# Performance work log

Hardware: AMD Instinct MI355X
Metric: run time of the kernel (lower is better)

Reference implementation:

```python
import math
import jax, jax.numpy as jnp
import numpy as np

N_NODES = 50000
N_EDGES = 400000
DIM = 64
HEADS = 4
GAMMA = 1.0
SIC_STRENGTH = 0.5


def _n2n(x):
    return jnp.nan_to_num(x, nan=0.0, posinf=0.0, neginf=0.0)


def _n2n_c(z):
    return jax.lax.complex(_n2n(z.real), _n2n(z.imag))


def setup_inputs() -> dict:
    key = jax.random.key(0)
    ks = jax.random.split(key, 8)
    scale = 1.0 / math.sqrt(DIM)  # ComplexLinear uniform(-1/sqrt(fan_in), 1/sqrt(fan_in))
    h_real = jax.random.normal(ks[0], (N_NODES, DIM), dtype=jnp.float32)
    h_imag = jax.random.normal(ks[1], (N_NODES, DIM), dtype=jnp.float32)
    W_real = jax.random.uniform(ks[2], (HEADS, DIM, DIM), minval=-scale, maxval=scale, dtype=jnp.float32)
    W_imag = jax.random.uniform(ks[3], (HEADS, DIM, DIM), minval=-scale, maxval=scale, dtype=jnp.float32)
    Q_real = jax.random.uniform(ks[4], (HEADS, DIM, DIM), minval=-scale, maxval=scale, dtype=jnp.float32)
    Q_imag = jax.random.uniform(ks[5], (HEADS, DIM, DIM), minval=-scale, maxval=scale, dtype=jnp.float32)
    msg_gate_raw = jnp.full((1,), 0.5, dtype=jnp.float32)  # _msg_gate init
    modrelu_b = jnp.zeros((DIM,), dtype=jnp.float32)
    src = jax.random.randint(ks[6], (N_EDGES,), 0, N_NODES, dtype=jnp.int32)
    dst = jax.random.randint(ks[7], (N_EDGES,), 0, N_NODES, dtype=jnp.int32)
    return {"h_real": h_real, "h_imag": h_imag, "W_real": W_real, "W_imag": W_imag,
            "Q_real": Q_real, "Q_imag": Q_imag, "msg_gate_raw": msg_gate_raw,
            "modrelu_b": modrelu_b, "src": src, "dst": dst}


def _segment_softmax(logits, seg, num_segments):
    # torch_geometric softmax: exp(x - max_seg) / (sum_seg + 1e-16)
    seg_max = jax.ops.segment_max(logits, seg, num_segments=num_segments)
    ex = jnp.exp(logits - seg_max[seg])
    denom = jax.ops.segment_sum(ex, seg, num_segments=num_segments)[seg] + 1e-16
    return ex / denom


def _forward(h_real, h_imag, W_real, W_imag, Q_real, Q_imag, msg_gate_raw, modrelu_b, src, dst):
    h = jax.lax.complex(h_real, h_imag)              # [N, D] complex64
    N, D = h.shape
    hs = h[src]                                      # [E, D] gather src
    hd = h[dst]                                      # [E, D] gather dst
    norm2 = jnp.clip(jnp.sum(hd.real ** 2 + hd.imag ** 2, axis=1, keepdims=True), 1e-6, None)
    gate = jax.nn.sigmoid(msg_gate_raw[0])

    # cosine similarity of real parts (detached), torch eps = 1e-8
    eps = 1e-8
    na = jnp.maximum(jnp.linalg.norm(hs.real, axis=-1), eps)
    nb = jnp.maximum(jnp.linalg.norm(hd.real, axis=-1), eps)
    sim = jnp.clip(jnp.sum(hs.real * hd.real, axis=-1) / (na * nb), -1.0, 1.0)
    sign = jax.lax.stop_gradient(jnp.sign(sim))      # [E]
    sign_gate = (0.5 + 0.5 * sign)[:, None]          # real factor applied to complex base

    updates = jnp.zeros((N, D), dtype=h.dtype)
    inv_sqrt_d = 1.0 / math.sqrt(D)
    for m in range(W_real.shape[0]):
        Wm = jax.lax.complex(W_real[m], W_imag[m])   # [D_out, D_in]
        Qm = jax.lax.complex(Q_real[m], Q_imag[m])
        Wh = _n2n_c(hs @ Wm.T)                       # transported, [E, D]
        dot = _n2n_c(jnp.sum(jnp.conj(hd) * Wh, axis=1, keepdims=True))
        proj = _n2n_c(hd * (dot / norm2))
        r = _n2n_c(Wh - SIC_STRENGTH * proj)
        Qh = _n2n_c(hd @ Qm.T)
        s = _n2n_c(jnp.sum(jnp.conj(Qh) * r, axis=1))
        logits = _n2n(GAMMA * jnp.abs(s) * inv_sqrt_d)
        alpha = _n2n(_segment_softmax(logits, dst, N))  # dropout is identity in eval
        base = _n2n_c((gate * r + (1.0 - gate) * Wh) * sign_gate)
        msg = _n2n_c(alpha[:, None] * base)
        updates = updates.at[dst].add(msg)

    h_new = _n2n_c(h + updates)
    # NodeNorm on view_as_real: mean/std over feature axis (dim=-2 of [N, D, 2]), ddof=1
    xr = jnp.stack([h_new.real, h_new.imag], axis=-1)          # [N, D, 2]
    mean = jnp.mean(xr, axis=-2, keepdims=True)
    std = jnp.clip(jnp.std(xr, axis=-2, ddof=1, keepdims=True), 1e-5, None)
    xn = _n2n((xr - mean) / std)
    h_new = jax.lax.complex(xn[..., 0], xn[..., 1])
    # ModReLU
    mag = jnp.clip(jnp.abs(h_new), 1e-6, None)
    gated = jax.nn.relu(mag + modrelu_b)
    out = _n2n_c(gated * (h_new / mag))
    return jnp.stack([out.real, out.imag], axis=-1)            # [N, D, 2] real view


def reference(h_real, h_imag, W_real, W_imag, Q_real, Q_imag, msg_gate_raw, modrelu_b, src, dst):
    return _forward(h_real, h_imag, W_real, W_imag, Q_real, Q_imag, msg_gate_raw, modrelu_b, src, dst)
```

## Files before the change

### kernel.cpp

```cpp
#include <hip/hip_runtime.h>
#include <hip/hip_bf16.h>
#include <math.h>

#define NN 50000
#define NE 400000
#define DIM 64
#define HEADS 4
#define SIC 0.5f
#define NBLK ((NN + 255) / 256)

typedef _Float16 f16x8 __attribute__((ext_vector_type(8)));
typedef _Float16 f16x2 __attribute__((ext_vector_type(2)));
typedef float f32x4 __attribute__((ext_vector_type(4)));

__device__ __forceinline__ unsigned pack_f16c(float re, float im) {
    f16x2 p; p[0] = (_Float16)re; p[1] = (_Float16)im;
    return __builtin_bit_cast(unsigned, p);
}

__device__ __forceinline__ f16x2 swapneg(f16x2 v) {
    unsigned u = __builtin_bit_cast(unsigned, v);
    u = ((u >> 16) | (u << 16)) ^ 0x8000u;
    return __builtin_bit_cast(f16x2, u);
}

__device__ __forceinline__ float dpp_red8(float x) {
    int xi = __builtin_bit_cast(int, x);
    x += __builtin_bit_cast(float, __builtin_amdgcn_update_dpp(0, xi, 0xB1, 0xF, 0xF, true));
    xi = __builtin_bit_cast(int, x);
    x += __builtin_bit_cast(float, __builtin_amdgcn_update_dpp(0, xi, 0x4E, 0xF, 0xF, true));
    xi = __builtin_bit_cast(int, x);
    x += __builtin_bit_cast(float, __builtin_amdgcn_update_dpp(0, xi, 0x141, 0xF, 0xF, true));
    return x;
}
__device__ __forceinline__ float dpp_red16(float x) {
    x = dpp_red8(x);
    int xi = __builtin_bit_cast(int, x);
    x += __builtin_bit_cast(float, __builtin_amdgcn_update_dpp(0, xi, 0x140, 0xF, 0xF, true));
    return x;
}

#define SA (512 * 128)
#define SB (SA + 512 * 128)
#define SC (SB + 128 * 512)
#define SD (SC + NN * 64)
#define SE (SD + NE)
__global__ void k_pre(const float* __restrict__ h_re, const float* __restrict__ h_im,
                      const float* __restrict__ Wre, const float* __restrict__ Wim,
                      const float* __restrict__ Qre, const float* __restrict__ Qim,
                      const int* __restrict__ dst,
                      _Float16* __restrict__ BtQ, _Float16* __restrict__ BtWH,
                      _Float16* __restrict__ B2f, unsigned* __restrict__ P16,
                      int* __restrict__ counts) {
    int tid = blockIdx.x * blockDim.x + threadIdx.x;
    if (tid < SA) {
        int c = tid >> 7, k = tid & 127;
        int mh = c >> 7, cm = c & 127;
        int comp = cm >> 6, o = cm & 63;
        int i = k >> 1, cin = k & 1;
        int widx = (mh * DIM + o) * DIM + i;
        float v;
        if (cin == 0) v = comp ? Qim[widx] : Qre[widx];
        else          v = comp ? Qre[widx] : -Qim[widx];
        BtQ[tid] = (_Float16)v;
    } else if (tid < SB) {
        int t2 = tid - SA;
        int c = t2 >> 7, k = t2 & 127;
        int mh = c >> 7, cm = c & 127;
        int comp = cm >> 6, o = cm & 63;
        int i = k >> 1, cin = k & 1;
        int widx = (mh * DIM + i) * DIM + o;
        float v;
        if (cin == 0) v = comp ? -Wim[widx] : Wre[widx];
        else          v = comp ?  Wre[widx] : Wim[widx];
        BtWH[t2] = (_Float16)v;
    } else if (tid < SC) {
        int t2 = tid - SB;
        int c_out = t2 >> 9, k = t2 & 511;
        int comp_out = c_out >> 6, o = c_out & 63;
        int m = k >> 7, cin = k & 1, i = (k >> 1) & 63;
        int widx = (m * DIM + o) * DIM + i;
        float v;
        if (cin == 0) v = comp_out ? Wim[widx] : Wre[widx];
        else          v = comp_out ? Wre[widx] : -Wim[widx];
        B2f[t2] = (_Float16)v;
    } else if (tid < SD) {
        int t2 = tid - SC;
        int n = t2 >> 6, d = t2 & 63;
        P16[t2] = pack_f16c(h_re[n * 64 + d], h_im[n * 64 + d]);
    } else if (tid < SE) {
        int e = tid - SD;
        atomicAdd(&counts[dst[e]], 1);
    }
}

__global__ __launch_bounds__(256) void k1f(
    const unsigned* __restrict__ P16, const _Float16* __restrict__ BtQ,
    const _Float16* __restrict__ BtWH, unsigned* __restrict__ W16) {
    __shared__ unsigned Qy[256 * 68];
    int b = blockIdx.x;
    int mh = b & 3, chunk = b >> 2;
    int w = threadIdx.x >> 6, l = threadIdx.x & 63;
    int r = l & 15, g = l >> 4;
    int nbase = chunk * 256;
    const _Float16* A = (const _Float16*)P16;

    {
        f16x8 Wf[2][4];
#pragma unroll
        for (int t = 0; t < 2; ++t)
#pragma unroll
            for (int ch = 0; ch < 4; ++ch)
                Wf[t][ch] = *(const f16x8*)(BtQ + (mh * 128 + t * 64 + w * 16 + r) * 128 + ch * 32 + g * 8);

        f16x8 N[3][4];
#pragma unroll
        for (int p = 0; p < 2; ++p) {
            int nc = min(nbase + p * 16 + r, NN - 1);
#pragma unroll
            for (int ch = 0; ch < 4; ++ch)
                N[p][ch] = *(const f16x8*)(A + (size_t)nc * 128 + ch * 32 + g * 8);
        }

#pragma unroll
        for (int nt = 0; nt < 16; ++nt) {
            const int cur = nt % 3;
            if (nt + 2 < 16) {
                const int nxt = (nt + 2) % 3;
                int nc = min(nbase + (nt + 2) * 16 + r, NN - 1);
#pragma unroll
                for (int ch = 0; ch < 4; ++ch)
                    N[nxt][ch] = *(const f16x8*)(A + (size_t)nc * 128 + ch * 32 + g * 8);
            }
            f32x4 a0 = {0.f, 0.f, 0.f, 0.f}, a1 = {0.f, 0.f, 0.f, 0.f};
#pragma unroll
            for (int ch = 0; ch < 4; ++ch) {
                a0 = __builtin_amdgcn_mfma_f32_16x16x32_f16(Wf[0][ch], N[cur][ch], a0, 0, 0, 0);
                a1 = __builtin_amdgcn_mfma_f32_16x16x32_f16(Wf[1][ch], N[cur][ch], a1, 0, 0, 0);
            }
            uint4 u;
            u.x = pack_f16c(a0[0], a1[0]);
            u.y = pack_f16c(a0[1], a1[1]);
            u.z = pack_f16c(a0[2], a1[2]);
            u.w = pack_f16c(a0[3], a1[3]);
            int node = nt * 16 + r;
            *(uint4*)&Qy[node * 68 + w * 16 + g * 4] = u;
        }
    }
    __syncthreads();

#pragma unroll 4
    for (int it = 0; it < 16; ++it) {
        int node = it * 16 + w * 4 + (l >> 4);
        int ll = l & 15, d0 = ll * 4;
        int n_glob = nbase + node;
        uint4 q = *(const uint4*)&Qy[node * 68 + d0];
        uint4 hp = make_uint4(0, 0, 0, 0);
        if (n_glob < NN) hp = *(const uint4*)&P16[(size_t)n_glob * 64 + d0];
        unsigned qw[4] = {q.x, q.y, q.z, q.w};
        unsigned hw[4] = {hp.x, hp.y, hp.z, hp.w};
        float qre[4], qim[4], hre[4], him[4];
        float tr = 0.f, ti = 0.f, n2 = 0.f;
#pragma unroll
        for (int j = 0; j < 4; ++j) {
            f16x2 pq = __builtin_bit_cast(f16x2, qw[j]);
            f16x2 ph = __builtin_bit_cast(f16x2, hw[j]);
            qre[j] = (float)pq[0]; qim[j] = (float)pq[1];
            hre[j] = (float)ph[0]; him[j] = (float)ph[1];
            tr += qre[j] * hre[j] + qim[j] * him[j];
            ti += qre[j] * him[j] - qim[j] * hre[j];
            n2 += hre[j] * hre[j] + him[j] * him[j];
        }
        tr = dpp_red16(tr); ti = dpp_red16(ti); n2 = dpp_red16(n2);
        float cfac = SIC / fmaxf(n2, 1e-6f);
        float kre = cfac * tr, kim = cfac * ti;
        uint4 y;
        unsigned* yp = &y.x;
#pragma unroll
        for (int j = 0; j < 4; ++j) {
            float yre = qre[j] - (kre * hre[j] + kim * him[j]);
            float yim = qim[j] - (kre * him[j] - kim * hre[j]);
            yp[j] = pack_f16c(yre, yim);
        }
        *(uint4*)&Qy[node * 68 + d0] = y;
    }
    __syncthreads();

    {
        f16x8 Wf[2][4];
#pragma unroll
        for (int t = 0; t < 2; ++t)
#pragma unroll
            for (int ch = 0; ch < 4; ++ch)
                Wf[t][ch] = *(const f16x8*)(BtWH + (mh * 128 + t * 64 + w * 16 + r) * 128 + ch * 32 + g * 8);

#pragma unroll
        for (int nt = 0; nt < 16; ++nt) {
            f32x4 a0 = {0.f, 0.f, 0.f, 0.f}, a1 = {0.f, 0.f, 0.f, 0.f};
#pragma unroll
            for (int ch = 0; ch < 4; ++ch) {
                f16x8 nf = *(const f16x8*)&Qy[(nt * 16 + r) * 68 + ch * 16 + g * 4];
                a0 = __builtin_amdgcn_mfma_f32_16x16x32_f16(Wf[0][ch], nf, a0, 0, 0, 0);
                a1 = __builtin_amdgcn_mfma_f32_16x16x32_f16(Wf[1][ch], nf, a1, 0, 0, 0);
            }
            int n = nbase + nt * 16 + r;
            if (n < NN) {
                uint4 u;
                u.x = pack_f16c(a0[0], a1[0]);
                u.y = pack_f16c(a0[1], a1[1]);
                u.z = pack_f16c(a0[2], a1[2]);
                u.w = pack_f16c(a0[3], a1[3]);
                *(uint4*)&W16[((size_t)n * 4 + mh) * 64 + w * 16 + g * 4] = u;
            }
        }
    }
}

__global__ __launch_bounds__(256) void k2b1(const int* __restrict__ counts,
                                            int* __restrict__ bsum) {
    __shared__ int red[256];
    int t = threadIdx.x;
    int i = blockIdx.x * 256 + t;
    red[t] = (i < NN) ? counts[i] : 0;
    __syncthreads();
    for (int off = 128; off; off >>= 1) {
        if (t < off) red[t] += red[t + off];
        __syncthreads();
    }
    if (t == 0) bsum[blockIdx.x] = red[0];
}

__global__ __launch_bounds__(256) void k2b2(const int* __restrict__ bsum,
                                            int* __restrict__ bpre) {
    __shared__ int buf[256];
    int t = threadIdx.x;
    int v = (t < NBLK) ? bsum[t] : 0;
    buf[t] = v;
    __syncthreads();
    for (int off = 1; off < 256; off <<= 1) {
        int x = 0;
        if (t >= off) x = buf[t - off];
        __syncthreads();
        buf[t] += x;
        __syncthreads();
    }
    if (t < NBLK) bpre[t] = buf[t] - v;
}

__global__ __launch_bounds__(256) void k2b3(const int* __restrict__ counts,
                                            const int* __restrict__ bpre,
                                            int* __restrict__ row_ptr, int* __restrict__ cursor) {
    __shared__ int buf[256];
    int t = threadIdx.x;
    int i = blockIdx.x * 256 + t;
    int v = (i < NN) ? counts[i] : 0;
    buf[t] = v;
    __syncthreads();
    for (int off = 1; off < 256; off <<= 1) {
        int x = 0;
        if (t >= off) x = buf[t - off];
        __syncthreads();
        buf[t] += x;
        __syncthreads();
    }
    int excl = buf[t] - v + bpre[blockIdx.x];
    if (i < NN) { row_ptr[i] = excl; cursor[i] = excl; }
    if (i == NN - 1) row_ptr[NN] = excl + v;
}

__global__ void k2c_fill(const int* __restrict__ src, const int* __restrict__ dst,
                         int* __restrict__ cursor, int* __restrict__ sorted_src) {
    int e = blockIdx.x * blockDim.x + threadIdx.x;
    if (e < NE) {
        int pos = atomicAdd(&cursor[dst[e]], 1);
        sorted_src[pos] = src[e] << 8;
    }
}

__global__ __launch_bounds__(128) void k_main(
    const float* __restrict__ h_re,
    const unsigned* __restrict__ P16,
    const unsigned* __restrict__ W16,
    const int* __restrict__ row_ptr, const int* __restrict__ sorted_src,
    _Float16* __restrict__ Sb) {
    int wave = threadIdx.x >> 6;
    int lane = threadIdx.x & 63;
    int n = blockIdx.x * 2 + wave;
    int e = lane >> 5;
    int g = (lane >> 3) & 3;
    int l = lane & 7;
    int d0 = l * 8;

    const char* hb = (const char*)h_re + d0 * 4;
    const char* pb = (const char*)P16 + d0 * 4;

    float hre[8];
    f16x2 w2[8], wn2[8];
    {
        float4 a0 = *(const float4*)(h_re + n * DIM + d0);
        float4 a1 = *(const float4*)(h_re + n * DIM + d0 + 4);
        hre[0] = a0.x; hre[1] = a0.y; hre[2] = a0.z; hre[3] = a0.w;
        hre[4] = a1.x; hre[5] = a1.y; hre[6] = a1.z; hre[7] = a1.w;
        const unsigned* wp = W16 + ((size_t)n * 4 + g) * 64 + d0;
        uint4 wa = *(const uint4*)wp, wb = *(const uint4*)(wp + 4);
        unsigned ww[8] = {wa.x, wa.y, wa.z, wa.w, wb.x, wb.y, wb.z, wb.w};
#pragma unroll
        for (int j = 0; j < 8; ++j) {
            w2[j] = __builtin_bit_cast(f16x2, ww[j]);
            wn2[j] = swapneg(w2[j]);
        }
    }

    int beg = row_ptr[n], end = row_ptr[n + 1];
    float l_run = 0.f;
    f16x2 ps[8];
#pragma unroll
    for (int j = 0; j < 8; ++j) ps[j] = f16x2{(_Float16)0.f, (_Float16)0.f};

    float4 aR0 = make_float4(0, 0, 0, 0), aR1 = aR0, bR0 = aR0, bR1 = aR0;
    uint4 aP0 = make_uint4(0, 0, 0, 0), aP1 = aP0, bP0 = aP0, bP1 = aP0;
    auto ldE = [&](int idx, float4& r0_, float4& r1_, uint4& p0_, uint4& p1_) {
        int soff = sorted_src[idx];
        r0_ = *(const float4*)(hb + soff);
        r1_ = *(const float4*)(hb + soff + 16);
        p0_ = *(const uint4*)(pb + soff);
        p1_ = *(const uint4*)(pb + soff + 16);
    };
    auto process = [&](const float4& R0, const float4& R1, const uint4& P0, const uint4& P1,
                       bool valid) {
        float csr[8] = {R0.x, R0.y, R0.z, R0.w, R1.x, R1.y, R1.z, R1.w};
        unsigned pw[8] = {P0.x, P0.y, P0.z, P0.w, P1.x, P1.y, P1.z, P1.w};
        float r2 = 0, r3 = 0, r4 = 0;
#pragma unroll
        for (int j = 0; j < 8; ++j) {
            f16x2 hs2 = __builtin_bit_cast(f16x2, pw[j]);
            r2 = __builtin_amdgcn_fdot2(w2[j], hs2, r2, false);
            r3 = __builtin_amdgcn_fdot2(wn2[j], hs2, r3, false);
            r4 = fmaf(hre[j], csr[j], r4);
        }
        r2 = dpp_red8(r2); r3 = dpp_red8(r3); r4 = dpp_red8(r4);

        float sg = (r4 > 0.f) ? 1.f : ((r4 < 0.f) ? 0.f : 0.5f);
        float mag2 = sqrtf(r2 * r2 + r3 * r3) * 0.180336880f;
        float ex = valid ? __builtin_exp2f(mag2) : 0.f;
        float wgt = fminf(ex * sg, 30000.f);
        l_run += ex;
        _Float16 wh = (_Float16)wgt;
        f16x2 wv = {wh, wh};
#pragma unroll
        for (int j = 0; j < 8; ++j) {
            f16x2 hs2 = __builtin_bit_cast(f16x2, pw[j]);
            ps[j] = ps[j] + wv * hs2;
        }
    };

    if (beg + e < end) ldE(beg + e, aR0, aR1, aP0, aP1);
    if (beg + 2 + e < end) ldE(beg + 2 + e, bR0, bR1, bP0, bP1);

    for (int pos = beg; pos < end; pos += 4) {
        process(aR0, aR1, aP0, aP1, (pos + e) < end);
        if (pos + 4 + e < end) ldE(pos + 4 + e, aR0, aR1, aP0, aP1);
        else { aR0 = make_float4(0, 0, 0, 0); aR1 = aR0; aP0 = make_uint4(0, 0, 0, 0); aP1 = aP0; }
        if (pos + 2 >= end) break;
        process(bR0, bR1, bP0, bP1, (pos + 2 + e) < end);
        if (pos + 6 + e < end) ldE(pos + 6 + e, bR0, bR1, bP0, bP1);
        else { bR0 = make_float4(0, 0, 0, 0); bR1 = bR0; bP0 = make_uint4(0, 0, 0, 0); bP1 = bP0; }
    }

#pragma unroll
    for (int j = 0; j < 8; ++j) {
        unsigned o = __shfl_xor(__builtin_bit_cast(unsigned, ps[j]), 32, 64);
        ps[j] = ps[j] + __builtin_bit_cast(f16x2, o);
    }
    l_run += __shfl_xor(l_run, 32, 64);

    float inv = (l_run > 0.f) ? (1.0f / l_run) : 0.f;
    if (e == 0) {
        _Float16 ih = (_Float16)inv;
        f16x2 iv = {ih, ih};
        uint4 o0, o1;
        unsigned* op0 = &o0.x;
        unsigned* op1 = &o1.x;
#pragma unroll
        for (int j = 0; j < 4; ++j) {
            op0[j] = __builtin_bit_cast(unsigned, (f16x2)(ps[j] * iv));
            op1[j] = __builtin_bit_cast(unsigned, (f16x2)(ps[j + 4] * iv));
        }
        _Float16* sp = Sb + (size_t)n * 512 + g * 128 + d0 * 2;
        *(uint4*)sp = o0;
        *(uint4*)(sp + 8) = o1;
    }
}

__global__ __launch_bounds__(256) void k5_ws(
    const float* __restrict__ h_re, const float* __restrict__ h_im,
    const _Float16* __restrict__ Sb,
    const _Float16* __restrict__ B2f,
    const float* __restrict__ gate_raw, const float* __restrict__ modrelu_b,
    float2* __restrict__ out) {
    int w = threadIdx.x >> 6, l = threadIdx.x & 63;
    int n0 = blockIdx.x * 64 + w * 16;
    if (n0 >= NN) return;
    int r = l & 15, g = l >> 4;
    int nodeA = min(n0 + r, NN - 1);

    f16x8 A_[16];
#pragma unroll
    for (int ch = 0; ch < 16; ++ch)
        A_[ch] = *(const f16x8*)(Sb + (size_t)nodeA * 512 + ch * 32 + g * 8);

    f16x8 Bf[8];
#pragma unroll
    for (int nt = 0; nt < 8; ++nt)
        Bf[nt] = *(const f16x8*)(B2f + (nt * 16 + r) * 512 + g * 8);

    f32x4 acc[8];
#pragma unroll
    for (int t = 0; t < 8; ++t) acc[t] = {0.f, 0.f, 0.f, 0.f};

#pragma unroll
    for (int ch = 0; ch < 16; ++ch) {
#pragma unroll
        for (int nt = 0; nt < 8; ++nt) {
            f16x8 b = Bf[nt];
            if (ch + 1 < 16)
                Bf[nt] = *(const f16x8*)(B2f + (nt * 16 + r) * 512 + (ch + 1) * 32 + g * 8);
            acc[nt] = __builtin_amdgcn_mfma_f32_16x16x32_f16(A_[ch], b, acc[nt], 0, 0, 0);
        }
    }

    float gate = 1.0f / (1.0f + expf(-gate_raw[0]));
    float bo[4];
#pragma unroll
    for (int q = 0; q < 4; ++q) bo[q] = modrelu_b[q * 16 + r];

#pragma unroll
    for (int j = 0; j < 4; ++j) {
        int n = n0 + g * 4 + j;
        int nc = min(n, NN - 1);
        float hrv[4], hiv[4];
        float tsr = 0.f, tsi = 0.f, hn2 = 0.f;
#pragma unroll
        for (int q = 0; q < 4; ++q) {
            int o = q * 16 + r;
            hrv[q] = h_re[nc * DIM + o];
            hiv[q] = h_im[nc * DIM + o];
            tsr += hrv[q] * acc[q][j] + hiv[q] * acc[q + 4][j];
            tsi += hrv[q] * acc[q + 4][j] - hiv[q] * acc[q][j];
            hn2 += hrv[q] * hrv[q] + hiv[q] * hiv[q];
        }
#pragma unroll
        for (int off = 1; off < 16; off <<= 1) {
            tsr += __shfl_xor(tsr, off, 64);
            tsi += __shfl_xor(tsi, off, 64);
            hn2 += __shfl_xor(hn2, off, 64);
        }
        float cfac = gate * SIC / fmaxf(hn2, 1e-6f);
        float Tsr = cfac * tsr, Tsi = cfac * tsi;

        float xr_[4], xi_[4];
        float sr = 0.f, si = 0.f, qr = 0.f, qi = 0.f;
#pragma unroll
        for (int q = 0; q < 4; ++q) {
            float hr = hrv[q], hi = hiv[q];
            float nre = hr + acc[q][j]     - (Tsr * hr - Tsi * hi);
            float nim = hi + acc[q + 4][j] - (Tsr * hi + Tsi * hr);
            xr_[q] = nre; xi_[q] = nim;
            sr += nre; si += nim; qr += nre * nre; qi += nim * nim;
        }
#pragma unroll
        for (int off = 1; off < 16; off <<= 1) {
            sr += __shfl_xor(sr, off, 64);
            si += __shfl_xor(si, off, 64);
            qr += __shfl_xor(qr, off, 64);
            qi += __shfl_xor(qi, off, 64);
        }
        float mean_r = sr * (1.f / DIM), mean_i = si * (1.f / DIM);
        float var_r = (qr - DIM * mean_r * mean_r) * (1.f / (DIM - 1));
        float var_i = (qi - DIM * mean_i * mean_i) * (1.f / (DIM - 1));
        float std_r = fmaxf(sqrtf(fmaxf(var_r, 0.f)), 1e-5f);
        float std_i = fmaxf(sqrtf(fmaxf(var_i, 0.f)), 1e-5f);
        if (n < NN) {
#pragma unroll
            for (int q = 0; q < 4; ++q) {
                float xr = (xr_[q] - mean_r) / std_r;
                float xi = (xi_[q] - mean_i) / std_i;
                float mag = fmaxf(sqrtf(xr * xr + xi * xi), 1e-6f);
                float gg = fmaxf(mag + bo[q], 0.f);
                float sc = gg / mag;
                out[n * DIM + q * 16 + r] = make_float2(xr * sc, xi * sc);
            }
        }
    }
}

extern "C" void kernel_launch(void* const* d_in, const int* in_sizes, int n_in,
                              void* d_out, int out_size, void* d_ws, size_t ws_size,
                              hipStream_t stream) {
    const float* h_re = (const float*)d_in[0];
    const float* h_im = (const float*)d_in[1];
    const float* W_re = (const float*)d_in[2];
    const float* W_im = (const float*)d_in[3];
    const float* Q_re = (const float*)d_in[4];
    const float* Q_im = (const float*)d_in[5];
    const float* gate_raw = (const float*)d_in[6];
    const float* b = (const float*)d_in[7];
    const int* src = (const int*)d_in[8];
    const int* dst = (const int*)d_in[9];

    char* ws = (char*)d_ws;
    size_t off = 0;
    auto alloc = [&](size_t bytes) {
        void* p = ws + off;
        off = (off + bytes + 255) & ~(size_t)255;
        return p;
    };
    _Float16* Sb = (_Float16*)alloc((size_t)NN * 512 * sizeof(_Float16));
    _Float16* BtQ = (_Float16*)alloc((size_t)512 * 128 * sizeof(_Float16));
    _Float16* BtWH = (_Float16*)alloc((size_t)512 * 128 * sizeof(_Float16));
    _Float16* B2f = (_Float16*)alloc((size_t)128 * 512 * sizeof(_Float16));
    unsigned* P16 = (unsigned*)alloc((size_t)NN * 64 * sizeof(unsigned));
    unsigned* W16 = (unsigned*)alloc((size_t)NN * 256 * sizeof(unsigned));
    int* counts = (int*)alloc((size_t)NN * sizeof(int));
    int* row_ptr = (int*)alloc((size_t)(NN + 1) * sizeof(int));
    int* cursor = (int*)alloc((size_t)NN * sizeof(int));
    int* sorted_src = (int*)alloc((size_t)NE * sizeof(int));
    int* bsum = (int*)alloc((size_t)NBLK * sizeof(int));
    int* bpre = (int*)alloc((size_t)(NBLK + 1) * sizeof(int));

    hipMemsetAsync(counts, 0, (size_t)NN * sizeof(int), stream);
    k_pre<<<(SE + 255) / 256, 256, 0, stream>>>(h_re, h_im, W_re, W_im, Q_re, Q_im, dst,
                                                BtQ, BtWH, B2f, P16, counts);
    k1f<<<4 * NBLK, 256, 0, stream>>>(P16, BtQ, BtWH, W16);
    k2b1<<<NBLK, 256, 0, stream>>>(counts, bsum);
    k2b2<<<1, 256, 0, stream>>>(bsum, bpre);
    k2b3<<<NBLK, 256, 0, stream>>>(counts, bpre, row_ptr, cursor);
    k2c_fill<<<(NE + 255) / 256, 256, 0, stream>>>(src, dst, cursor, sorted_src);
    k_main<<<NN / 2, 128, 0, stream>>>(h_re, P16, W16, row_ptr, sorted_src, Sb);
    k5_ws<<<(NN + 63) / 64, 256, 0, stream>>>(h_re, h_im, Sb, B2f, gate_raw, b, (float2*)d_out);
}
```

Measured before the change: 262.0 us.

## Split k5 output columns across wave pairs and pre-swizzle B2 for coalesced loads

```diff
diff --git a/kernel.cpp b/kernel.cpp
--- a/kernel.cpp
+++ b/kernel.cpp
@@ -50,7 +50,7 @@
                       const float* __restrict__ Qre, const float* __restrict__ Qim,
                       const int* __restrict__ dst,
                       _Float16* __restrict__ BtQ, _Float16* __restrict__ BtWH,
-                      _Float16* __restrict__ B2f, unsigned* __restrict__ P16,
+                      _Float16* __restrict__ B2c, unsigned* __restrict__ P16,
                       int* __restrict__ counts) {
     int tid = blockIdx.x * blockDim.x + threadIdx.x;
     if (tid < SA) {
@@ -76,14 +76,20 @@
         BtWH[t2] = (_Float16)v;
     } else if (tid < SC) {
         int t2 = tid - SB;
-        int c_out = t2 >> 9, k = t2 & 511;
+        int ch = t2 >> 12;
+        int rem = t2 & 4095;
+        int nt = rem >> 9;
+        int rem2 = rem & 511;
+        int slot = rem2 >> 3, j = rem2 & 7;
+        int c_out = nt * 16 + (slot >> 2);
+        int k = ch * 32 + (slot & 3) * 8 + j;
         int comp_out = c_out >> 6, o = c_out & 63;
         int m = k >> 7, cin = k & 1, i = (k >> 1) & 63;
         int widx = (m * DIM + o) * DIM + i;
         float v;
         if (cin == 0) v = comp_out ? Wim[widx] : Wre[widx];
         else          v = comp_out ? Wre[widx] : -Wim[widx];
-        B2f[t2] = (_Float16)v;
+        B2c[t2] = (_Float16)v;
     } else if (tid < SD) {
         int t2 = tid - SC;
         int n = t2 >> 6, d = t2 & 63;
@@ -395,59 +401,77 @@
 __global__ __launch_bounds__(256) void k5_ws(
     const float* __restrict__ h_re, const float* __restrict__ h_im,
     const _Float16* __restrict__ Sb,
-    const _Float16* __restrict__ B2f,
+    const _Float16* __restrict__ B2c,
     const float* __restrict__ gate_raw, const float* __restrict__ modrelu_b,
     float2* __restrict__ out) {
+    __shared__ float xch[2][32][8];
     int w = threadIdx.x >> 6, l = threadIdx.x & 63;
-    int n0 = blockIdx.x * 64 + w * 16;
-    if (n0 >= NN) return;
     int r = l & 15, g = l >> 4;
+    int nh = w >> 1, ct = w & 1;
+    int nbase = blockIdx.x * 32;
+    int n0 = nbase + nh * 16;
     int nodeA = min(n0 + r, NN - 1);
-
-    f16x8 A_[16];
-#pragma unroll
-    for (int ch = 0; ch < 16; ++ch)
-        A_[ch] = *(const f16x8*)(Sb + (size_t)nodeA * 512 + ch * 32 + g * 8);
-
-    f16x8 Bf[8];
-#pragma unroll
-    for (int nt = 0; nt < 8; ++nt)
-        Bf[nt] = *(const f16x8*)(B2f + (nt * 16 + r) * 512 + g * 8);
-
-    f32x4 acc[8];
-#pragma unroll
-    for (int t = 0; t < 8; ++t) acc[t] = {0.f, 0.f, 0.f, 0.f};
-
+    int q0 = 2 * ct;
+    const int nt_[4] = {q0, q0 + 1, 4 + q0, 5 + q0};
+    int slot8 = ((r << 2) + g) << 3;
+
+    const _Float16* abase = Sb + (size_t)nodeA * 512 + g * 8;
+    const _Float16* bbase = B2c + slot8;
+
+    f32x4 acc[4];
+#pragma unroll
+    for (int t = 0; t < 4; ++t) acc[t] = {0.f, 0.f, 0.f, 0.f};
+
+    f16x8 Ac = *(const f16x8*)(abase);
+    f16x8 Bc0 = *(const f16x8*)(bbase + nt_[0] * 512);
+    f16x8 Bc1 = *(const f16x8*)(bbase + nt_[1] * 512);
+    f16x8 Bc2 = *(const f16x8*)(bbase + nt_[2] * 512);
+    f16x8 Bc3 = *(const f16x8*)(bbase + nt_[3] * 512);
 #pragma unroll
     for (int ch = 0; ch < 16; ++ch) {
-#pragma unroll
-        for (int nt = 0; nt < 8; ++nt) {
-            f16x8 b = Bf[nt];
-            if (ch + 1 < 16)
-                Bf[nt] = *(const f16x8*)(B2f + (nt * 16 + r) * 512 + (ch + 1) * 32 + g * 8);
-            acc[nt] = __builtin_amdgcn_mfma_f32_16x16x32_f16(A_[ch], b, acc[nt], 0, 0, 0);
-        }
+        f16x8 An = Ac, Bn0 = Bc0, Bn1 = Bc1, Bn2 = Bc2, Bn3 = Bc3;
+        if (ch + 1 < 16) {
+            An = *(const f16x8*)(abase + (ch + 1) * 32);
+            const _Float16* bn = bbase + (ch + 1) * 4096;
+            Bn0 = *(const f16x8*)(bn + nt_[0] * 512);
+            Bn1 = *(const f16x8*)(bn + nt_[1] * 512);
+            Bn2 = *(const f16x8*)(bn + nt_[2] * 512);
+            Bn3 = *(const f16x8*)(bn + nt_[3] * 512);
+        }
+        acc[0] = __builtin_amdgcn_mfma_f32_16x16x32_f16(Ac, Bc0, acc[0], 0, 0, 0);
+        acc[1] = __builtin_amdgcn_mfma_f32_16x16x32_f16(Ac, Bc1, acc[1], 0, 0, 0);
+        acc[2] = __builtin_amdgcn_mfma_f32_16x16x32_f16(Ac, Bc2, acc[2], 0, 0, 0);
+        acc[3] = __builtin_amdgcn_mfma_f32_16x16x32_f16(Ac, Bc3, acc[3], 0, 0, 0);
+        Ac = An; Bc0 = Bn0; Bc1 = Bn1; Bc2 = Bn2; Bc3 = Bn3;
     }
 
     float gate = 1.0f / (1.0f + expf(-gate_raw[0]));
-    float bo[4];
-#pragma unroll
-    for (int q = 0; q < 4; ++q) bo[q] = modrelu_b[q * 16 + r];
-
+    float bo[2];
+#pragma unroll
+    for (int qq = 0; qq < 2; ++qq) bo[qq] = modrelu_b[(q0 + qq) * 16 + r];
+
+    float hr[4][2], hi[4][2];
 #pragma unroll
     for (int j = 0; j < 4; ++j) {
-        int n = n0 + g * 4 + j;
-        int nc = min(n, NN - 1);
-        float hrv[4], hiv[4];
+        int nc = min(n0 + g * 4 + j, NN - 1);
+#pragma unroll
+        for (int qq = 0; qq < 2; ++qq) {
+            int o = (q0 + qq) * 16 + r;
+            hr[j][qq] = h_re[nc * DIM + o];
+            hi[j][qq] = h_im[nc * DIM + o];
+        }
+    }
+
+    float tsr_p[4], tsi_p[4], hn2_p[4];
+#pragma unroll
+    for (int j = 0; j < 4; ++j) {
         float tsr = 0.f, tsi = 0.f, hn2 = 0.f;
 #pragma unroll
-        for (int q = 0; q < 4; ++q) {
-            int o = q * 16 + r;
-            hrv[q] = h_re[nc * DIM + o];
-            hiv[q] = h_im[nc * DIM + o];
-            tsr += hrv[q] * acc[q][j] + hiv[q] * acc[q + 4][j];
-            tsi += hrv[q] * acc[q + 4][j] - hiv[q] * acc[q][j];
-            hn2 += hrv[q] * hrv[q] + hiv[q] * hiv[q];
+        for (int qq = 0; qq < 2; ++qq) {
+            float ur = acc[qq][j], ui = acc[2 + qq][j];
+            tsr += hr[j][qq] * ur + hi[j][qq] * ui;
+            tsi += hr[j][qq] * ui - hi[j][qq] * ur;
+            hn2 += hr[j][qq] * hr[j][qq] + hi[j][qq] * hi[j][qq];
         }
 #pragma unroll
         for (int off = 1; off < 16; off <<= 1) {
@@ -455,17 +479,38 @@
             tsi += __shfl_xor(tsi, off, 64);
             hn2 += __shfl_xor(hn2, off, 64);
         }
+        tsr_p[j] = tsr; tsi_p[j] = tsi; hn2_p[j] = hn2;
+        if (r == 0) {
+            int nloc = nh * 16 + g * 4 + j;
+            xch[ct][nloc][0] = tsr;
+            xch[ct][nloc][1] = tsi;
+            xch[ct][nloc][2] = hn2;
+        }
+    }
+    __syncthreads();
+
+    float Tsr[4], Tsi[4];
+#pragma unroll
+    for (int j = 0; j < 4; ++j) {
+        int nloc = nh * 16 + g * 4 + j;
+        float tsr = tsr_p[j] + xch[1 - ct][nloc][0];
+        float tsi = tsi_p[j] + xch[1 - ct][nloc][1];
+        float hn2 = hn2_p[j] + xch[1 - ct][nloc][2];
         float cfac = gate * SIC / fmaxf(hn2, 1e-6f);
-        float Tsr = cfac * tsr, Tsi = cfac * tsi;
-
-        float xr_[4], xi_[4];
+        Tsr[j] = cfac * tsr; Tsi[j] = cfac * tsi;
+    }
+
+    float xr_[4][2], xi_[4][2];
+    float sr_p[4], si_p[4], qr_p[4], qi_p[4];
+#pragma unroll
+    for (int j = 0; j < 4; ++j) {
         float sr = 0.f, si = 0.f, qr = 0.f, qi = 0.f;
 #pragma unroll
-        for (int q = 0; q < 4; ++q) {
-            float hr = hrv[q], hi = hiv[q];
-            float nre = hr + acc[q][j]     - (Tsr * hr - Tsi * hi);
-            float nim = hi + acc[q + 4][j] - (Tsr * hi + Tsi * hr);
-            xr_[q] = nre; xi_[q] = nim;
+        for (int qq = 0; qq < 2; ++qq) {
+            float hrv = hr[j][qq], hiv = hi[j][qq];
+            float nre = hrv + acc[qq][j]     - (Tsr[j] * hrv - Tsi[j] * hiv);
+            float nim = hiv + acc[2 + qq][j] - (Tsr[j] * hiv + Tsi[j] * hrv);
+            xr_[j][qq] = nre; xi_[j][qq] = nim;
             sr += nre; si += nim; qr += nre * nre; qi += nim * nim;
         }
 #pragma unroll
@@ -475,6 +520,25 @@
             qr += __shfl_xor(qr, off, 64);
             qi += __shfl_xor(qi, off, 64);
         }
+        sr_p[j] = sr; si_p[j] = si; qr_p[j] = qr; qi_p[j] = qi;
+        if (r == 0) {
+            int nloc = nh * 16 + g * 4 + j;
+            xch[ct][nloc][4] = sr;
+            xch[ct][nloc][5] = si;
+            xch[ct][nloc][6] = qr;
+            xch[ct][nloc][7] = qi;
+        }
+    }
+    __syncthreads();
+
+#pragma unroll
+    for (int j = 0; j < 4; ++j) {
+        int nloc = nh * 16 + g * 4 + j;
+        int n = n0 + g * 4 + j;
+        float sr = sr_p[j] + xch[1 - ct][nloc][4];
+        float si = si_p[j] + xch[1 - ct][nloc][5];
+        float qr = qr_p[j] + xch[1 - ct][nloc][6];
+        float qi = qi_p[j] + xch[1 - ct][nloc][7];
         float mean_r = sr * (1.f / DIM), mean_i = si * (1.f / DIM);
         float var_r = (qr - DIM * mean_r * mean_r) * (1.f / (DIM - 1));
         float var_i = (qi - DIM * mean_i * mean_i) * (1.f / (DIM - 1));
@@ -482,13 +546,13 @@
         float std_i = fmaxf(sqrtf(fmaxf(var_i, 0.f)), 1e-5f);
         if (n < NN) {
 #pragma unroll
-            for (int q = 0; q < 4; ++q) {
-                float xr = (xr_[q] - mean_r) / std_r;
-                float xi = (xi_[q] - mean_i) / std_i;
+            for (int qq = 0; qq < 2; ++qq) {
+                float xr = (xr_[j][qq] - mean_r) / std_r;
+                float xi = (xi_[j][qq] - mean_i) / std_i;
                 float mag = fmaxf(sqrtf(xr * xr + xi * xi), 1e-6f);
-                float gg = fmaxf(mag + bo[q], 0.f);
+                float gg = fmaxf(mag + bo[qq], 0.f);
                 float sc = gg / mag;
-                out[n * DIM + q * 16 + r] = make_float2(xr * sc, xi * sc);
+                out[n * DIM + (q0 + qq) * 16 + r] = make_float2(xr * sc, xi * sc);
             }
         }
     }
@@ -518,7 +582,7 @@
     _Float16* Sb = (_Float16*)alloc((size_t)NN * 512 * sizeof(_Float16));
     _Float16* BtQ = (_Float16*)alloc((size_t)512 * 128 * sizeof(_Float16));
     _Float16* BtWH = (_Float16*)alloc((size_t)512 * 128 * sizeof(_Float16));
-    _Float16* B2f = (_Float16*)alloc((size_t)128 * 512 * sizeof(_Float16));
+    _Float16* B2c = (_Float16*)alloc((size_t)128 * 512 * sizeof(_Float16));
     unsigned* P16 = (unsigned*)alloc((size_t)NN * 64 * sizeof(unsigned));
     unsigned* W16 = (unsigned*)alloc((size_t)NN * 256 * sizeof(unsigned));
     int* counts = (int*)alloc((size_t)NN * sizeof(int));
@@ -530,12 +594,12 @@
 
     hipMemsetAsync(counts, 0, (size_t)NN * sizeof(int), stream);
     k_pre<<<(SE + 255) / 256, 256, 0, stream>>>(h_re, h_im, W_re, W_im, Q_re, Q_im, dst,
-                                                BtQ, BtWH, B2f, P16, counts);
+                                                BtQ, BtWH, B2c, P16, counts);
     k1f<<<4 * NBLK, 256, 0, stream>>>(P16, BtQ, BtWH, W16);
     k2b1<<<NBLK, 256, 0, stream>>>(counts, bsum);
     k2b2<<<1, 256, 0, stream>>>(bsum, bpre);
     k2b3<<<NBLK, 256, 0, stream>>>(counts, bpre, row_ptr, cursor);
     k2c_fill<<<(NE + 255) / 256, 256, 0, stream>>>(src, dst, cursor, sorted_src);
     k_main<<<NN / 2, 128, 0, stream>>>(h_re, P16, W16, row_ptr, sorted_src, Sb);
-    k5_ws<<<(NN + 63) / 64, 256, 0, stream>>>(h_re, h_im, Sb, B2f, gate_raw, b, (float2*)d_out);
-}
+    k5_ws<<<(NN + 31) / 32, 256, 0, stream>>>(h_re, h_im, Sb, B2c, gate_raw, b, (float2*)d_out);
+}
```

Result: faster. 237.5 us (-9.4%).
